# Optimization experiments

Measured on AMD Instinct MI355X. Metric: run time of the kernel, lower is better.

The kernel has to match this reference:

```python
import jax, jax.numpy as jnp
import numpy as np

C = 64
CQK = C // 8  # query/key channels = 8


def setup_inputs() -> dict:
    key = jax.random.key(0)
    ks = jax.random.split(key, 7)
    B, D, H, W = 1, 16, 32, 32
    x = jax.random.normal(ks[0], (B, C, D, H, W), dtype=jnp.float32)
    # 1x1x1 Conv3d weights collapse to [out_ch, in_ch] matrices; std=0.01 per nn.init.normal_
    wq = 0.01 * jax.random.normal(ks[1], (CQK, C), dtype=jnp.float32)
    bq = jnp.zeros((CQK,), dtype=jnp.float32)
    wk = 0.01 * jax.random.normal(ks[2], (CQK, C), dtype=jnp.float32)
    bk = jnp.zeros((CQK,), dtype=jnp.float32)
    wv = 0.01 * jax.random.normal(ks[3], (C, C), dtype=jnp.float32)
    bv = jnp.zeros((C,), dtype=jnp.float32)
    gamma = jnp.zeros((1,), dtype=jnp.float32)  # nn.Parameter(torch.zeros(1))
    return {"x": x, "wq": wq, "bq": bq, "wk": wk, "bk": bk, "wv": wv, "bv": bv, "gamma": gamma}


def reference(x, wq, bq, wk, bk, wv, bv, gamma):
    B, Cc, D, H, W = x.shape
    N = D * H * W
    xf = x.reshape(B, Cc, N)  # [B, C, N]
    # 1x1x1 convs == per-position linear projections
    q = jnp.einsum('oc,bcn->bon', wq, xf) + bq[None, :, None]   # [B, CQK, N]
    k = jnp.einsum('oc,bcn->bon', wk, xf) + bk[None, :, None]   # [B, CQK, N]
    v = jnp.einsum('oc,bcn->bon', wv, xf) + bv[None, :, None]   # [B, C, N]
    # attention[b, i, j] = softmax_j( q[:, :, i] . k[:, :, j] )  -> [B, N, N]
    scores = jnp.einsum('bon,bom->bnm', q, k)
    attn = jax.nn.softmax(scores, axis=-1)
    # out[b, c, i] = sum_j v[b, c, j] * attn[b, i, j]
    out = jnp.einsum('bcm,bnm->bcn', v, attn).reshape(B, Cc, D, H, W)
    return x + gamma * out
```

## Files before the change

### kernel.cpp

```cpp
#include <hip/hip_runtime.h>

#define NPOS 16384
#define KSPLIT 8
#define KEYS_PER_BLK (NPOS / KSPLIT)
#define CHUNK 512
#define LOG2E 1.4426950408889634f

typedef short bf16x8 __attribute__((ext_vector_type(8)));
typedef unsigned short u16x8 __attribute__((ext_vector_type(8)));
typedef float floatx16 __attribute__((ext_vector_type(16)));
typedef float floatx2 __attribute__((ext_vector_type(2)));

static __device__ __forceinline__ unsigned short f2bf(float f) {
    return (unsigned short)(__builtin_bit_cast(unsigned int, f) >> 16);
}
static __device__ __forceinline__ float bf2f(unsigned short h) {
    return __builtin_bit_cast(float, (unsigned int)h << 16);
}

#if __has_builtin(__builtin_amdgcn_exp2f)
static __device__ __forceinline__ float exp2_fast(float x) {
    return __builtin_amdgcn_exp2f(x);
}
#else
static __device__ __forceinline__ float exp2_fast(float x) {
    float r;
    asm("v_exp_f32 %0, %1" : "=v"(r) : "v"(x));
    return r;
}
#endif

static __device__ __forceinline__ unsigned int pk_bf16(float e_even, float e_odd) {
    return __builtin_amdgcn_perm(__builtin_bit_cast(unsigned int, e_odd),
                                 __builtin_bit_cast(unsigned int, e_even),
                                 0x07060302u);
}

static __device__ __forceinline__ int sigma(int n) {
    const int w12 = n & 12;
    return (w12 == 4 || w12 == 8) ? (n ^ 12) : n;
}

__global__ __launch_bounds__(256) void proj_kernel(
    const float* __restrict__ x,
    const float* __restrict__ wq, const float* __restrict__ bq,
    const float* __restrict__ wk, const float* __restrict__ bk,
    const float* __restrict__ wv, const float* __restrict__ bv,
    unsigned short* __restrict__ qb16, unsigned short* __restrict__ kb16,
    unsigned short* __restrict__ vbg16)
{
    const int t = threadIdx.x;
    const int n = blockIdx.x * 256 + t;
    const int g = blockIdx.y;

    const float* w;
    const float* b;
    if (g == 0)      { w = wq; b = bq; }
    else if (g == 1) { w = wk; b = bk; }
    else             { w = wv + (g - 2) * 8 * 64; b = bv + (g - 2) * 8; }

    float acc[8];
#pragma unroll
    for (int oo = 0; oo < 8; ++oo) acc[oo] = b[oo];
#pragma unroll 16
    for (int c = 0; c < 64; ++c) {
        const float xv = x[c * NPOS + n];
#pragma unroll
        for (int oo = 0; oo < 8; ++oo)
            acc[oo] = fmaf(w[oo * 64 + c], xv, acc[oo]);
    }

    if (g == 0) {
        u16x8 qp;
#pragma unroll
        for (int j = 0; j < 8; ++j) qp[j] = f2bf(acc[j] * LOG2E);
        ((uint4*)qb16)[n] = __builtin_bit_cast(uint4, qp);
    } else if (g == 1) {
        u16x8 kp;
#pragma unroll
        for (int j = 0; j < 8; ++j) kp[j] = f2bf(acc[j]);
        ((uint4*)kb16)[n] = __builtin_bit_cast(uint4, kp);
    } else {
        const int o0 = (g - 2) * 8;
        const int np = sigma(n);
        const size_t base = (size_t)(np >> 3) * 512 + (np & 7);
#pragma unroll
        for (int oo = 0; oo < 8; ++oo)
            vbg16[base + (size_t)(o0 + oo) * 8] = f2bf(acc[oo]);
    }
}

__global__ __launch_bounds__(256, 4) void attn_kernel(
    const uint4* __restrict__ qb4,
    const uint4* __restrict__ kb4,
    const uint4* __restrict__ vbg4,
    unsigned short* __restrict__ nump,
    float* __restrict__ denp)
{
    __shared__ __align__(16) char smem[8448];
    uint4* k_lds = (uint4*)smem;

    const int t     = threadIdx.x;
    const int wave  = t >> 6;
    const int lane  = t & 63;
    const int m     = lane & 31;
    const int half  = lane >> 5;
    const int qhalf = wave >> 1;
    const int khalf = wave & 1;

    const int qblk = blockIdx.x >> 3;
    const int kq   = blockIdx.x & 7;
    const int i0   = qblk * 64;
    const int jb   = kq * KEYS_PER_BLK;

    if (t == 0) k_lds[512] = make_uint4(0, 0, 0, 0);

    uint4 qa4 = (half == 0) ? qb4[i0 + qhalf * 32 + m] : make_uint4(0, 0, 0, 0);
    const bf16x8 bqf = __builtin_bit_cast(bf16x8, qa4);

    floatx16 accA = {};
    floatx16 accB = {};
    floatx2  dacc2 = {0.f, 0.f};

#pragma unroll 1
    for (int c4 = 0; c4 < 4; ++c4) {
        const int j0 = jb + c4 * CHUNK;
        __syncthreads();
        k_lds[t]       = kb4[j0 + t];
        k_lds[256 + t] = kb4[j0 + 256 + t];
        __syncthreads();

        const int kwb = khalf * 256;
#pragma unroll 2
        for (int st = 0; st < 8; ++st) {
            const int kb_ = kwb + st * 32;
            const bf16x8 ak = __builtin_bit_cast(
                bf16x8, k_lds[half ? 512 : (kb_ + m)]);
            const floatx16 s = __builtin_amdgcn_mfma_f32_32x32x16_bf16(
                ak, bqf, (floatx16){}, 0, 0, 0);

            float e[16];
#pragma unroll
            for (int r = 0; r < 16; ++r) e[r] = exp2_fast(s[r]);
#pragma unroll
            for (int p = 0; p < 8; ++p)
                dacc2 += (floatx2){e[2 * p], e[2 * p + 1]};
            unsigned int P[8];
#pragma unroll
            for (int p = 0; p < 8; ++p) P[p] = pk_bf16(e[2 * p], e[2 * p + 1]);

            const int g8t = (j0 + kb_) >> 3;
#pragma unroll
            for (int f = 0; f < 2; ++f) {
                uint4 afu;
                afu.x = P[4 * f + 0];
                afu.y = P[4 * f + 1];
                afu.z = P[4 * f + 2];
                afu.w = P[4 * f + 3];
                const bf16x8 af = __builtin_bit_cast(bf16x8, afu);

                const int g8 = g8t + f * 2 + half;
                const bf16x8 v0 = __builtin_bit_cast(
                    bf16x8, vbg4[(size_t)g8 * 64 + m]);
                const bf16x8 v1 = __builtin_bit_cast(
                    bf16x8, vbg4[(size_t)g8 * 64 + 32 + m]);
                accA = __builtin_amdgcn_mfma_f32_32x32x16_bf16(af, v0, accA,
                                                               0, 0, 0);
                accB = __builtin_amdgcn_mfma_f32_32x32x16_bf16(af, v1, accB,
                                                               0, 0, 0);
            }
        }
    }

    const float dl = dacc2[0] + dacc2[1];
    const float dw = dl + __shfl_xor(dl, 32);

    __syncthreads();
    float*          xden = (float*)smem;
    unsigned short* xacc = (unsigned short*)(smem + 256);
    const int recl = qhalf * 64 + lane;
    if (khalf == 1) {
        if (half == 0) xden[qhalf * 32 + m] = dw;
        u16x8 a0, a1, a2, a3;
#pragma unroll
        for (int j = 0; j < 8; ++j) {
            a0[j] = f2bf(accA[j]);
            a1[j] = f2bf(accA[8 + j]);
            a2[j] = f2bf(accB[j]);
            a3[j] = f2bf(accB[8 + j]);
        }
        uint4* dst = (uint4*)(xacc + recl * 32);
        dst[0] = __builtin_bit_cast(uint4, a0);
        dst[1] = __builtin_bit_cast(uint4, a1);
        dst[2] = __builtin_bit_cast(uint4, a2);
        dst[3] = __builtin_bit_cast(uint4, a3);
    }
    __syncthreads();
    if (khalf == 0) {
        const uint4* src = (const uint4*)(xacc + recl * 32);
        const u16x8 b0 = __builtin_bit_cast(u16x8, src[0]);
        const u16x8 b1 = __builtin_bit_cast(u16x8, src[1]);
        const u16x8 b2 = __builtin_bit_cast(u16x8, src[2]);
        const u16x8 b3 = __builtin_bit_cast(u16x8, src[3]);
        u16x8 o0, o1, o2, o3;
#pragma unroll
        for (int j = 0; j < 8; ++j) {
            o0[j] = f2bf(accA[j]      + bf2f(b0[j]));
            o1[j] = f2bf(accA[8 + j]  + bf2f(b1[j]));
            o2[j] = f2bf(accB[j]      + bf2f(b2[j]));
            o3[j] = f2bf(accB[8 + j]  + bf2f(b3[j]));
        }
        const size_t base =
            ((((size_t)kq * 256 + qblk) * 2 + qhalf) * 64 + lane) * 32;
        uint4* gdst = (uint4*)(nump + base);
        gdst[0] = __builtin_bit_cast(uint4, o0);
        gdst[1] = __builtin_bit_cast(uint4, o1);
        gdst[2] = __builtin_bit_cast(uint4, o2);
        gdst[3] = __builtin_bit_cast(uint4, o3);
        if (half == 0)
            denp[(size_t)kq * NPOS + i0 + qhalf * 32 + m] =
                dw + xden[qhalf * 32 + m];
    }
}

__global__ __launch_bounds__(256) void finalize_kernel(
    const float* __restrict__ x,
    const unsigned short* __restrict__ nump,
    const float* __restrict__ denp,
    const float* __restrict__ gamma,
    float* __restrict__ out)
{
    const int idx  = blockIdx.x * 256 + threadIdx.x;
    const int n    = idx & (NPOS - 1);
    const int c    = idx >> 14;
    const int qblk = n >> 6;
    const int qh   = (n >> 5) & 1;
    const int row  = n & 31;
    const int hf   = (row >> 2) & 1;
    const int r    = (row & 3) + 4 * (row >> 3);
    const int lane = (c & 31) + 32 * hf;
    const int off  = ((c >> 5) << 4) + r;

    float ns = 0.f, ds = 0.f;
#pragma unroll
    for (int kq = 0; kq < 8; ++kq) {
        const size_t rec =
            ((((size_t)kq * 256 + qblk) * 2 + qh) * 64 + lane) * 32 + off;
        ns += bf2f(nump[rec]);
        ds += denp[(size_t)kq * NPOS + n];
    }
    out[idx] = fmaf(gamma[0], ns * __builtin_amdgcn_rcpf(ds), x[idx]);
}

extern "C" void kernel_launch(void* const* d_in, const int* in_sizes, int n_in,
                              void* d_out, int out_size, void* d_ws, size_t ws_size,
                              hipStream_t stream)
{
    (void)in_sizes; (void)n_in; (void)out_size; (void)ws_size;

    const float* x     = (const float*)d_in[0];
    const float* wq    = (const float*)d_in[1];
    const float* bq    = (const float*)d_in[2];
    const float* wk    = (const float*)d_in[3];
    const float* bk    = (const float*)d_in[4];
    const float* wv    = (const float*)d_in[5];
    const float* bv    = (const float*)d_in[6];
    const float* gamma = (const float*)d_in[7];
    float* out = (float*)d_out;

    char* ws = (char*)d_ws;
    unsigned short* qb16  = (unsigned short*)(ws);
    unsigned short* kb16  = (unsigned short*)(ws + 262144);
    unsigned short* vbg16 = (unsigned short*)(ws + 524288);
    unsigned short* nump  = (unsigned short*)(ws + 2621440);
    float*          denp  = (float*)(ws + 19398656);

    proj_kernel<<<dim3(NPOS / 256, 10), 256, 0, stream>>>(
        x, wq, bq, wk, bk, wv, bv, qb16, kb16, vbg16);
    attn_kernel<<<(NPOS / 64) * KSPLIT, 256, 0, stream>>>(
        (const uint4*)qb16, (const uint4*)kb16, (const uint4*)vbg16,
        nump, denp);
    finalize_kernel<<<(64 * NPOS) / 256, 256, 0, stream>>>(x, nump, denp,
                                                           gamma, out);
}
```

Measured before the change: 140.2 us.

## Vectorize finalize reads per record and raise attention occupancy bound

The finalize kernel is reorganised so each block handles one 32-query half-block record. Each thread loads 8 contiguous bf16 partials as one 16-byte vector instead of scattered 2-byte loads. The denominators are reduced once into shared memory with atomics. The attention kernel also raises its launch-bounds minimum blocks from 4 to 6 and stops unrolling the inner key loop, which trades instruction-level parallelism for occupancy and risks register spills. The finalize output writes become strided per thread and may coalesce less well.

```diff
diff --git a/kernel.cpp b/kernel.cpp
--- a/kernel.cpp
+++ b/kernel.cpp
@@ -90,7 +90,7 @@
     }
 }
 
-__global__ __launch_bounds__(256, 4) void attn_kernel(
+__global__ __launch_bounds__(256, 6) void attn_kernel(
     const uint4* __restrict__ qb4,
     const uint4* __restrict__ kb4,
     const uint4* __restrict__ vbg4,
@@ -131,7 +131,7 @@
         __syncthreads();
 
         const int kwb = khalf * 256;
-#pragma unroll 2
+#pragma unroll 1
         for (int st = 0; st < 8; ++st) {
             const int kb_ = kwb + st * 32;
             const bf16x8 ak = __builtin_bit_cast(
@@ -230,26 +230,46 @@
     const float* __restrict__ gamma,
     float* __restrict__ out)
 {
-    const int idx  = blockIdx.x * 256 + threadIdx.x;
-    const int n    = idx & (NPOS - 1);
-    const int c    = idx >> 14;
-    const int qblk = n >> 6;
-    const int qh   = (n >> 5) & 1;
-    const int row  = n & 31;
-    const int hf   = (row >> 2) & 1;
-    const int r    = (row & 3) + 4 * (row >> 3);
-    const int lane = (c & 31) + 32 * hf;
-    const int off  = ((c >> 5) << 4) + r;
-
-    float ns = 0.f, ds = 0.f;
+    const int b    = blockIdx.x;
+    const int qblk = b >> 1;
+    const int qh   = b & 1;
+    const int t    = threadIdx.x;
+    const int lane = t >> 2;
+    const int u    = t & 3;
+    const int n0   = qblk * 64 + qh * 32;
+
+    __shared__ float dsum[32];
+    if (t < 32) dsum[t] = 0.f;
+    __syncthreads();
+    atomicAdd(&dsum[t & 31], denp[(size_t)(t >> 5) * NPOS + n0 + (t & 31)]);
+    __syncthreads();
+
+    float ns[8];
+#pragma unroll
+    for (int j = 0; j < 8; ++j) ns[j] = 0.f;
 #pragma unroll
     for (int kq = 0; kq < 8; ++kq) {
-        const size_t rec =
-            ((((size_t)kq * 256 + qblk) * 2 + qh) * 64 + lane) * 32 + off;
-        ns += bf2f(nump[rec]);
-        ds += denp[(size_t)kq * NPOS + n];
-    }
-    out[idx] = fmaf(gamma[0], ns * __builtin_amdgcn_rcpf(ds), x[idx]);
+        const size_t base =
+            ((((size_t)kq * 256 + qblk) * 2 + qh) * 64 + lane) * 32 + u * 8;
+        const u16x8 h = __builtin_bit_cast(u16x8, *(const uint4*)(nump + base));
+#pragma unroll
+        for (int j = 0; j < 8; ++j) ns[j] += bf2f(h[j]);
+    }
+
+    const float g     = gamma[0];
+    const int   clow  = lane & 31;
+    const int   hf    = lane >> 5;
+    const int   chigh = u >> 1;
+    const int   c     = chigh * 32 + clow;
+#pragma unroll
+    for (int j = 0; j < 8; ++j) {
+        const int off = u * 8 + j;
+        const int r   = off & 15;
+        const int row = (r & 3) + 8 * (r >> 2) + 4 * hf;
+        const int n   = n0 + row;
+        const size_t gi = (size_t)c * NPOS + n;
+        out[gi] = fmaf(g, ns[j] * __builtin_amdgcn_rcpf(dsum[row]), x[gi]);
+    }
 }
 
 extern "C" void kernel_launch(void* const* d_in, const int* in_sizes, int n_in,
@@ -280,6 +300,5 @@
     attn_kernel<<<(NPOS / 64) * KSPLIT, 256, 0, stream>>>(
         (const uint4*)qb16, (const uint4*)kb16, (const uint4*)vbg16,
         nump, denp);
-    finalize_kernel<<<(64 * NPOS) / 256, 256, 0, stream>>>(x, nump, denp,
-                                                           gamma, out);
-}
+    finalize_kernel<<<512, 256, 0, stream>>>(x, nump, denp, gamma, out);
+}
```

After: 141.4 us. About the same (+0.8%).
